# Kernel optimization log

Measured on AMD Instinct MI355X. Metric: run time of the kernel, lower is better.

The kernel has to match this reference:

```python
import jax, jax.numpy as jnp
import numpy as np

B, DIM, H, W = 2, 384, 256, 256
HID = DIM * 1          # ffn_expansion_factor = 1 (required for source code to be consistent)
P = 8                  # patch_size


def setup_inputs() -> dict:
    key = jax.random.key(0)
    k0, k1, k2, k3, k4 = jax.random.split(key, 5)
    x = jax.random.normal(k0, (B, DIM, H, W), jnp.float32)
    # learned spectral filter: (hidden, P, P//2+1), real-valued, multiplies rfft2 coeffs
    fft_filter = jax.random.normal(k1, (HID, P, P // 2 + 1), jnp.float32)
    # project_in: 1x1 conv dim->hidden, weight (out,in)
    w_in = jax.random.normal(k2, (HID, DIM), jnp.float32) * (1.0 / np.sqrt(DIM))
    # depthwise 3x3 conv, groups=channels, weight (C,1,3,3)
    w_dw = jax.random.normal(k3, (HID, 1, 3, 3), jnp.float32) * (1.0 / 3.0)
    # project_out: 1x1 conv hidden//2 -> dim
    w_out = jax.random.normal(k4, (DIM, HID // 2), jnp.float32) * (1.0 / np.sqrt(HID // 2))
    return {"x": x, "fft_filter": fft_filter, "w_in": w_in, "w_dw": w_dw, "w_out": w_out}


def reference(x, fft_filter, w_in, w_dw, w_out):
    b, c, h, w = x.shape
    hid = w_in.shape[0]
    hb, wb = h // P, w // P
    # project_in (1x1 conv == channel GEMM)
    t = jnp.einsum('bchw,oc->bohw', x, w_in)
    # patchify into 8x8 blocks and apply per-patch 2D real FFT spectral filter.
    # reshape b c (hb p1) (wb p2) -> b c hb p1 wb p2; FFT over axes (3,5).
    tp = t.reshape(b, hid, hb, P, wb, P)
    tf = jnp.fft.rfft2(tp, axes=(3, 5))                 # (b,hid,hb,P,wb,P//2+1) complex
    tf = tf * fft_filter[None, :, None, :, None, :]
    tp = jnp.fft.irfft2(tf, s=(P, P), axes=(3, 5))
    t = tp.reshape(b, hid, h, w)
    # depthwise 3x3 conv, stride 1, padding 1
    t = jax.lax.conv_general_dilated(
        t, w_dw, window_strides=(1, 1), padding='SAME',
        feature_group_count=hid,
        dimension_numbers=('NCHW', 'OIHW', 'NCHW'))
    # gated GELU (exact erf gelu, matching torch F.gelu default)
    x1, x2 = t[:, : hid // 2], t[:, hid // 2:]
    g = jax.nn.gelu(x1, approximate=False) * x2
    # project_out (1x1 conv)
    return jnp.einsum('bchw,oc->bohw', g, w_out)
```

## Files before the change

kernel.cpp:

```cpp
#include <hip/hip_runtime.h>
#include <hip/hip_bf16.h>
#include <math.h>

#define BB 2
#define DIM 384
#define HID 384
#define HW 65536

typedef short s16x8 __attribute__((ext_vector_type(8)));
typedef short s16x4 __attribute__((ext_vector_type(4)));
typedef __bf16 bf16x8 __attribute__((ext_vector_type(8)));
typedef float f32x4 __attribute__((ext_vector_type(4)));

__device__ inline short f2b(float f) {
    __hip_bfloat16 h = __float2bfloat16(f);
    return __builtin_bit_cast(short, h);
}
__device__ inline float b2f(short s) {
    return __bfloat162float(__builtin_bit_cast(__hip_bfloat16, s));
}

__device__ inline void gl_lds16(const short* g, short* l) {
    __builtin_amdgcn_global_load_lds(
        (const __attribute__((address_space(1))) unsigned int*)g,
        (__attribute__((address_space(3))) unsigned int*)l, 16, 0, 0);
}

__global__ void k_prepR(short* __restrict__ Rb) {
    int idx = blockIdx.x * 256 + threadIdx.x;
    int j = idx >> 6, k = idx & 63;
    const float cas[8] = {1.f, 1.41421356237f, 1.f, 0.f, -1.f, -1.41421356237f, -1.f, 0.f};
    int t = ((j >> 3) * (k >> 3) + (j & 7) * (k & 7)) & 7;
    Rb[idx] = f2b(cas[t]);
}

__global__ void k_prepD(const float* __restrict__ F, float* __restrict__ Dt) {
    int idx = blockIdx.x * 256 + threadIdx.x;
    int c = idx >> 6, j = idx & 63;
    int a = j >> 3, q = j & 7;
    float d;
    if (q >= 1 && q <= 3)
        d = F[c * 40 + a * 5 + q];
    else if (q >= 5)
        d = F[c * 40 + ((8 - a) & 7) * 5 + (8 - q)];
    else
        d = 0.5f * (F[c * 40 + a * 5 + q] + F[c * 40 + ((8 - a) & 7) * 5 + q]);
    Dt[j * 384 + c] = d * (1.f / 64.f);
}

__global__ void k_cvtw(const float* __restrict__ in, short* __restrict__ out, int n) {
    int i = blockIdx.x * 256 + threadIdx.x;
    if (i < n) out[i] = f2b(in[i]);
}

__global__ __launch_bounds__(256) void k_cvtx(const float* __restrict__ X, short* __restrict__ Xt) {
    int hw0 = blockIdx.x * 64, c0 = blockIdx.y * 64, b = blockIdx.z;
    __shared__ __align__(16) short S[64 * 64];
    int t = threadIdx.x;
    const float* Xb = X + ((size_t)(b * DIM) << 16);
    short* Xtb = Xt + (size_t)b * HW * DIM;
#pragma unroll
    for (int p = 0; p < 2; ++p) {
        int row = p * 32 + (t >> 3), sb = t & 7;
        const float* src = &Xb[((size_t)(c0 + row) << 16) + hw0 + sb * 8];
        float4 a = *(const float4*)src;
        float4 bq = *(const float4*)(src + 4);
        s16x8 v;
        v[0] = f2b(a.x);  v[1] = f2b(a.y);  v[2] = f2b(a.z);  v[3] = f2b(a.w);
        v[4] = f2b(bq.x); v[5] = f2b(bq.y); v[6] = f2b(bq.z); v[7] = f2b(bq.w);
        *(s16x8*)&S[row * 64 + ((sb ^ (row >> 3)) << 3)] = v;
    }
    __syncthreads();
#pragma unroll
    for (int p = 0; p < 2; ++p) {
        int row = p * 32 + (t >> 3), ch = t & 7;
        s16x8 v;
#pragma unroll
        for (int j = 0; j < 8; ++j)
            v[j] = S[(ch * 8 + j) * 64 + (row ^ (ch << 3))];
        *(s16x8*)&Xtb[(size_t)(hw0 + row) * DIM + c0 + ch * 8] = v;
    }
}

__global__ __launch_bounds__(256) void k_gemm1c(const short* __restrict__ A,
                                                const short* __restrict__ Bt,
                                                const short* __restrict__ Rb,
                                                const float* __restrict__ Dt,
                                                short* __restrict__ T) {
    __shared__ __align__(16) short SH[17408 + 4096];
    short* As = SH;
    short* Bs = SH + 4096;
    short* Rs = SH + 17408;
    int d = blockIdx.x;
    int wg = (d & 7) * 192 + (d >> 3);
    int m0 = (wg % 3) * 128;
    int tx = wg / 3;
    int h0 = (tx >> 4) * 8;
    int w0 = (tx & 15) * 16;
    int b  = blockIdx.z;
    const short* Bz = Bt + (size_t)b * HW * DIM;
    int tid = threadIdx.x;
    int lane = tid & 63, w = tid >> 6;
    int wr = w >> 1, wc = w & 1;
    int lm = lane & 15, quad = lane >> 4;

    {
        int j0 = tid >> 3, kb0 = tid & 7;
        gl_lds16(Rb + j0 * 64 + ((kb0 ^ (j0 & 7)) << 3), Rs + tid * 8);
        int t2 = tid + 256;
        int j1 = t2 >> 3, kb1 = t2 & 7;
        gl_lds16(Rb + j1 * 64 + ((kb1 ^ (j1 & 7)) << 3), Rs + t2 * 8);
    }

    f32x4 acc[4][4];
#pragma unroll
    for (int i = 0; i < 4; ++i)
#pragma unroll
        for (int j = 0; j < 4; ++j) acc[i][j] = 0.f;

    int srow = tid >> 2, sseg = tid & 3;
    int pu = srow >> 3, pv = srow & 7;
    int p1 = ((h0 + pu) << 8) + w0 + pv;
    int p2 = p1 + 8;
    for (int k0 = 0; k0 < DIM; k0 += 32) {
        gl_lds16(A + (size_t)(m0 + srow) * DIM + k0 + sseg * 8, As + tid * 8);
        gl_lds16(A + (size_t)(m0 + 64 + srow) * DIM + k0 + sseg * 8, As + (tid + 256) * 8);
        gl_lds16(Bz + (size_t)p1 * DIM + k0 + sseg * 8, Bs + tid * 8);
        gl_lds16(Bz + (size_t)p2 * DIM + k0 + sseg * 8, Bs + (tid + 256) * 8);
        __syncthreads();
        bf16x8 af[4], bfr[4];
#pragma unroll
        for (int i = 0; i < 4; ++i)
            af[i] = __builtin_bit_cast(bf16x8, *(const s16x8*)&As[(wr * 64 + i * 16 + lm) * 32 + quad * 8]);
#pragma unroll
        for (int j = 0; j < 4; ++j)
            bfr[j] = __builtin_bit_cast(bf16x8, *(const s16x8*)&Bs[(wc * 64 + j * 16 + lm) * 32 + quad * 8]);
#pragma unroll
        for (int i = 0; i < 4; ++i)
#pragma unroll
            for (int j = 0; j < 4; ++j)
                acc[i][j] = __builtin_amdgcn_mfma_f32_16x16x32_bf16(af[i], bfr[j], acc[i][j], 0, 0, 0);
        __syncthreads();
    }
#pragma unroll
    for (int i = 0; i < 4; ++i)
#pragma unroll
        for (int j = 0; j < 4; ++j)
#pragma unroll
            for (int r = 0; r < 4; ++r)
                SH[(wr * 64 + i * 16 + quad * 4 + r) * 136 + wc * 64 + j * 16 + lm] =
                    f2b(acc[i][j][r]);
    __syncthreads();

    f32x4 acc2[4][4];
#pragma unroll
    for (int i = 0; i < 4; ++i)
#pragma unroll
        for (int j = 0; j < 4; ++j) acc2[i][j] = 0.f;
#pragma unroll
    for (int ks = 0; ks < 2; ++ks) {
        bf16x8 af[4], bfr[4];
#pragma unroll
        for (int i = 0; i < 4; ++i)
            af[i] = __builtin_bit_cast(bf16x8,
                *(const s16x8*)&SH[(wr * 64 + i * 16 + lm) * 136 + wc * 64 + ks * 32 + quad * 8]);
#pragma unroll
        for (int jf = 0; jf < 4; ++jf)
            bfr[jf] = __builtin_bit_cast(bf16x8,
                *(const s16x8*)&Rs[(jf * 16 + lm) * 64 + (((ks * 4 + quad) ^ (lm & 7)) << 3)]);
#pragma unroll
        for (int i = 0; i < 4; ++i)
#pragma unroll
            for (int jf = 0; jf < 4; ++jf)
                acc2[i][jf] = __builtin_amdgcn_mfma_f32_16x16x32_bf16(af[i], bfr[jf], acc2[i][jf], 0, 0, 0);
    }
#pragma unroll
    for (int i = 0; i < 4; ++i)
#pragma unroll
        for (int jf = 0; jf < 4; ++jf) {
            int j = jf * 16 + lm;
            float4 dv = *(const float4*)&Dt[j * 384 + m0 + wr * 64 + i * 16 + quad * 4];
            acc2[i][jf][0] *= dv.x; acc2[i][jf][1] *= dv.y;
            acc2[i][jf][2] *= dv.z; acc2[i][jf][3] *= dv.w;
        }
    __syncthreads();
#pragma unroll
    for (int i = 0; i < 4; ++i)
#pragma unroll
        for (int jf = 0; jf < 4; ++jf)
#pragma unroll
            for (int r = 0; r < 4; ++r)
                SH[(wr * 64 + i * 16 + quad * 4 + r) * 136 + wc * 64 + jf * 16 + lm] =
                    f2b(acc2[i][jf][r]);
    __syncthreads();

    f32x4 acc3[4][4];
#pragma unroll
    for (int i = 0; i < 4; ++i)
#pragma unroll
        for (int j = 0; j < 4; ++j) acc3[i][j] = 0.f;
#pragma unroll
    for (int ks = 0; ks < 2; ++ks) {
        bf16x8 af[4], bfr[4];
#pragma unroll
        for (int i = 0; i < 4; ++i)
            af[i] = __builtin_bit_cast(bf16x8,
                *(const s16x8*)&SH[(wr * 64 + i * 16 + lm) * 136 + wc * 64 + ks * 32 + quad * 8]);
#pragma unroll
        for (int uf = 0; uf < 4; ++uf)
            bfr[uf] = __builtin_bit_cast(bf16x8,
                *(const s16x8*)&Rs[(uf * 16 + lm) * 64 + (((ks * 4 + quad) ^ (lm & 7)) << 3)]);
#pragma unroll
        for (int i = 0; i < 4; ++i)
#pragma unroll
            for (int uf = 0; uf < 4; ++uf)
                acc3[i][uf] = __builtin_amdgcn_mfma_f32_16x16x32_bf16(af[i], bfr[uf], acc3[i][uf], 0, 0, 0);
    }
    __syncthreads();
#pragma unroll
    for (int i = 0; i < 4; ++i)
#pragma unroll
        for (int uf = 0; uf < 4; ++uf)
#pragma unroll
            for (int r = 0; r < 4; ++r)
                SH[(wr * 64 + i * 16 + quad * 4 + r) * 136 + wc * 64 + uf * 16 + lm] =
                    f2b(acc3[i][uf][r]);
    __syncthreads();
#pragma unroll
    for (int kq = 0; kq < 8; ++kq) {
        int idx = kq * 256 + tid;
        int pat = idx & 1, ch = (idx >> 1) & 127, u = idx >> 8;
        s16x8 vv = *(const s16x8*)&SH[ch * 136 + pat * 64 + u * 8];
        *(s16x8*)&T[(((size_t)(b * HID + m0 + ch)) << 16) + ((h0 + u) << 8) + w0 + pat * 8] = vv;
    }
}

__global__ __launch_bounds__(256) void k_dwgt(const short* __restrict__ Y,
                                              const float* __restrict__ Wdw,
                                              short* __restrict__ Gt) {
    int bz = blockIdx.z;
    int b  = bz / 24;
    int cg = bz % 24;
    int c0 = cg * 8;
    int h0 = blockIdx.y * 16, w0 = blockIdx.x * 64;
    __shared__ __align__(16) short S[16][18][80];
    __shared__ float sw[16][9];
    int tid = threadIdx.x;
    if (tid < 144) {
        int p = tid / 9, j = tid % 9;
        int ch = (p < 8) ? (c0 + p) : (c0 + p - 8 + 192);
        sw[p][j] = Wdw[ch * 9 + j];
    }
    for (int t = tid; t < 2880; t += 256) {
        int v = t % 10, r = (t / 10) % 18, p = t / 180;
        int gh = h0 + r - 1;
        int gw = w0 + v * 8 - 8;
        int ch = (p < 8) ? (c0 + p) : (c0 + p - 8 + 192);
        s16x8 val = {0, 0, 0, 0, 0, 0, 0, 0};
        if (gh >= 0 && gh < 256 && gw >= 0 && gw <= 248)
            val = *(const s16x8*)&Y[((size_t)(b * HID + ch) << 16) + (gh << 8) + gw];
        *(s16x8*)&S[p][r][v * 8] = val;
    }
    __syncthreads();
    s16x8 ov[4];
#pragma unroll
    for (int it = 0; it < 4; ++it) {
        int idx = it * 256 + tid;
        int p = idx >> 7, run = idx & 127;
        int r = run >> 3, c8 = (run & 7) * 8;
        float z1[8], z2[8];
#pragma unroll
        for (int k = 0; k < 8; ++k) { z1[k] = 0.f; z2[k] = 0.f; }
#pragma unroll
        for (int i = 0; i < 3; ++i) {
            {
                s16x4 wv[4];
#pragma unroll
                for (int q = 0; q < 4; ++q) wv[q] = *(const s16x4*)&S[p][r + i][c8 + 4 + q * 4];
                float fv[10];
#pragma unroll
                for (int q = 0; q < 10; ++q) fv[q] = b2f(wv[(q + 3) >> 2][(q + 3) & 3]);
#pragma unroll
                for (int j = 0; j < 3; ++j) {
                    float wgt = sw[p][i * 3 + j];
#pragma unroll
                    for (int k = 0; k < 8; ++k) z1[k] += fv[k + j] * wgt;
                }
            }
            {
                s16x4 wv[4];
#pragma unroll
                for (int q = 0; q < 4; ++q) wv[q] = *(const s16x4*)&S[p + 8][r + i][c8 + 4 + q * 4];
                float fv[10];
#pragma unroll
                for (int q = 0; q < 10; ++q) fv[q] = b2f(wv[(q + 3) >> 2][(q + 3) & 3]);
#pragma unroll
                for (int j = 0; j < 3; ++j) {
                    float wgt = sw[p + 8][i * 3 + j];
#pragma unroll
                    for (int k = 0; k < 8; ++k) z2[k] += fv[k + j] * wgt;
                }
            }
        }
#pragma unroll
        for (int k = 0; k < 8; ++k) {
            float g = 0.5f * z1[k] * (1.f + erff(z1[k] * 0.70710678118654752f));
            ov[it][k] = f2b(g * z2[k]);
        }
    }
    __syncthreads();
    short* Ob = (short*)S;
#pragma unroll
    for (int it = 0; it < 4; ++it) {
        int idx = it * 256 + tid;
        int p = idx >> 7, run = idx & 127;
        int pos = (run >> 3) * 64 + (run & 7) * 8;
#pragma unroll
        for (int k = 0; k < 8; ++k)
            Ob[(pos + k) * 9 + p] = ov[it][k];
    }
    __syncthreads();
    short* Gb = Gt + (((size_t)(b * 24 + cg)) << 16) * 8;
#pragma unroll
    for (int it = 0; it < 4; ++it) {
        int pos = it * 256 + tid;
        int r = pos >> 6, cl = pos & 63;
        s16x8 v;
#pragma unroll
        for (int k = 0; k < 8; ++k) v[k] = Ob[pos * 9 + k];
        *(s16x8*)&Gb[(size_t)(((h0 + r) << 8) + w0 + cl) * 8] = v;
    }
}

__global__ __launch_bounds__(256) void k_gemm_bf16(const short* __restrict__ A,
                                                   const short* __restrict__ Bt,
                                                   float* __restrict__ C,
                                                   int N, int K) {
    __shared__ __align__(16) short As[128 * 32];
    __shared__ __align__(16) short Bs[128 * 32];
    const short* Bz = Bt + (size_t)blockIdx.z * (size_t)N * K;
    float* Cz = C + (size_t)blockIdx.z * (size_t)384 * N;
    int d = blockIdx.x;
    int wg = (d & 7) * 192 + (d >> 3);
    int m0 = (wg % 3) * 128;
    int n0 = (wg / 3) * 128;
    int tid = threadIdx.x;
    int lane = tid & 63, w = tid >> 6;
    int wr = w >> 1, wc = w & 1;
    int lm = lane & 15, quad = lane >> 4;

    f32x4 acc[4][4];
#pragma unroll
    for (int i = 0; i < 4; ++i)
#pragma unroll
        for (int j = 0; j < 4; ++j) acc[i][j] = 0.f;

    int srow = tid >> 2, sseg = tid & 3;
    for (int k0 = 0; k0 < K; k0 += 32) {
        gl_lds16(A + (size_t)(m0 + srow) * K + k0 + sseg * 8, As + tid * 8);
        gl_lds16(A + (size_t)(m0 + 64 + srow) * K + k0 + sseg * 8, As + (tid + 256) * 8);
        gl_lds16(Bz + ((size_t)((k0 >> 3) + sseg) * HW + n0 + srow) * 8, Bs + tid * 8);
        gl_lds16(Bz + ((size_t)((k0 >> 3) + sseg) * HW + n0 + 64 + srow) * 8, Bs + (tid + 256) * 8);
        __syncthreads();
        bf16x8 af[4], bfr[4];
#pragma unroll
        for (int i = 0; i < 4; ++i)
            af[i] = __builtin_bit_cast(bf16x8, *(const s16x8*)&As[(wr * 64 + i * 16 + lm) * 32 + quad * 8]);
#pragma unroll
        for (int j = 0; j < 4; ++j)
            bfr[j] = __builtin_bit_cast(bf16x8, *(const s16x8*)&Bs[(wc * 64 + j * 16 + lm) * 32 + quad * 8]);
#pragma unroll
        for (int i = 0; i < 4; ++i)
#pragma unroll
            for (int j = 0; j < 4; ++j)
                acc[i][j] = __builtin_amdgcn_mfma_f32_16x16x32_bf16(af[i], bfr[j], acc[i][j], 0, 0, 0);
        __syncthreads();
    }
#pragma unroll
    for (int i = 0; i < 4; ++i) {
        int r0 = m0 + wr * 64 + i * 16 + quad * 4;
#pragma unroll
        for (int j = 0; j < 4; ++j) {
            int cidx = n0 + wc * 64 + j * 16 + lm;
#pragma unroll
            for (int r = 0; r < 4; ++r)
                Cz[(size_t)(r0 + r) * N + cidx] = acc[i][j][r];
        }
    }
}

extern "C" void kernel_launch(void* const* d_in, const int* in_sizes, int n_in,
                              void* d_out, int out_size, void* d_ws, size_t ws_size,
                              hipStream_t stream) {
    const float* x     = (const float*)d_in[0];
    const float* ff    = (const float*)d_in[1];
    const float* w_in  = (const float*)d_in[2];
    const float* w_dw  = (const float*)d_in[3];
    const float* w_out = (const float*)d_in[4];
    float* out = (float*)d_out;

    char* ws = (char*)d_ws;
    float* Dt   = (float*)ws;
    short* wbin = (short*)(ws + 98304);
    short* wbout = (short*)(ws + 393216);
    short* Rbuf = (short*)(ws + 540672);
    short* bufA = (short*)(ws + 548864);
    short* bufB = (short*)(ws + 548864 + (size_t)100663296);
    short* Gt = bufA;

    k_prepR<<<16, 256, 0, stream>>>(Rbuf);
    k_prepD<<<96, 256, 0, stream>>>(ff, Dt);
    k_cvtw<<<(DIM * DIM + 255) / 256, 256, 0, stream>>>(w_in, wbin, DIM * DIM);
    k_cvtw<<<(DIM * 192 + 255) / 256, 256, 0, stream>>>(w_out, wbout, DIM * 192);
    k_cvtx<<<dim3(HW / 64, DIM / 64, BB), 256, 0, stream>>>(x, bufA);

    k_gemm1c<<<dim3(1536, 1, BB), 256, 0, stream>>>(wbin, bufA, Rbuf, Dt, bufB);

    k_dwgt<<<dim3(4, 16, BB * 24), 256, 0, stream>>>(bufB, w_dw, Gt);

    k_gemm_bf16<<<dim3(1536, 1, BB), 256, 0, stream>>>(wbout, Gt, out, HW, 192);
}
```

Measured before the change: 599.6 us.

## Store filtered intermediate patch-major, drop intra-warp barriers, merge prep kernels

The spectral-filter GEMM kernel now writes its bf16 output in a patch-major layout (each 8x8 patch contiguous), so every channel row's store is one contiguous 256-byte run. The depthwise-conv kernel's loads are re-indexed to match. Four __syncthreads between the staged MFMA passes are removed, because each warp only reads back the shared-memory tile region it wrote itself. The four small weight and table prep kernels are merged into one launch to cut launch overhead. The risk is that the halo loads in the depthwise kernel now come from scattered patch rows, which may reduce coalescing there.

```diff
diff --git a/kernel.cpp b/kernel.cpp
--- a/kernel.cpp
+++ b/kernel.cpp
@@ -26,31 +26,35 @@
         (__attribute__((address_space(3))) unsigned int*)l, 16, 0, 0);
 }
 
-__global__ void k_prepR(short* __restrict__ Rb) {
-    int idx = blockIdx.x * 256 + threadIdx.x;
-    int j = idx >> 6, k = idx & 63;
-    const float cas[8] = {1.f, 1.41421356237f, 1.f, 0.f, -1.f, -1.41421356237f, -1.f, 0.f};
-    int t = ((j >> 3) * (k >> 3) + (j & 7) * (k & 7)) & 7;
-    Rb[idx] = f2b(cas[t]);
-}
-
-__global__ void k_prepD(const float* __restrict__ F, float* __restrict__ Dt) {
-    int idx = blockIdx.x * 256 + threadIdx.x;
-    int c = idx >> 6, j = idx & 63;
-    int a = j >> 3, q = j & 7;
-    float d;
-    if (q >= 1 && q <= 3)
-        d = F[c * 40 + a * 5 + q];
-    else if (q >= 5)
-        d = F[c * 40 + ((8 - a) & 7) * 5 + (8 - q)];
-    else
-        d = 0.5f * (F[c * 40 + a * 5 + q] + F[c * 40 + ((8 - a) & 7) * 5 + q]);
-    Dt[j * 384 + c] = d * (1.f / 64.f);
-}
-
-__global__ void k_cvtw(const float* __restrict__ in, short* __restrict__ out, int n) {
+__global__ void k_prep(const float* __restrict__ w_in, const float* __restrict__ w_out,
+                       const float* __restrict__ F,
+                       short* __restrict__ wbin, short* __restrict__ wbout,
+                       float* __restrict__ Dt, short* __restrict__ Rb) {
     int i = blockIdx.x * 256 + threadIdx.x;
-    if (i < n) out[i] = f2b(in[i]);
+    if (i < 147456) { wbin[i] = f2b(w_in[i]); return; }
+    i -= 147456;
+    if (i < 73728) { wbout[i] = f2b(w_out[i]); return; }
+    i -= 73728;
+    if (i < 24576) {
+        int c = i >> 6, j = i & 63;
+        int a = j >> 3, q = j & 7;
+        float d;
+        if (q >= 1 && q <= 3)
+            d = F[c * 40 + a * 5 + q];
+        else if (q >= 5)
+            d = F[c * 40 + ((8 - a) & 7) * 5 + (8 - q)];
+        else
+            d = 0.5f * (F[c * 40 + a * 5 + q] + F[c * 40 + ((8 - a) & 7) * 5 + q]);
+        Dt[j * 384 + c] = d * (1.f / 64.f);
+        return;
+    }
+    i -= 24576;
+    if (i < 4096) {
+        int j = i >> 6, k = i & 63;
+        const float cas[8] = {1.f, 1.41421356237f, 1.f, 0.f, -1.f, -1.41421356237f, -1.f, 0.f};
+        int t = ((j >> 3) * (k >> 3) + (j & 7) * (k & 7)) & 7;
+        Rb[i] = f2b(cas[t]);
+    }
 }
 
 __global__ __launch_bounds__(256) void k_cvtx(const float* __restrict__ X, short* __restrict__ Xt) {
@@ -150,7 +154,6 @@
             for (int r = 0; r < 4; ++r)
                 SH[(wr * 64 + i * 16 + quad * 4 + r) * 136 + wc * 64 + j * 16 + lm] =
                     f2b(acc[i][j][r]);
-    __syncthreads();
 
     f32x4 acc2[4][4];
 #pragma unroll
@@ -183,7 +186,6 @@
             acc2[i][jf][0] *= dv.x; acc2[i][jf][1] *= dv.y;
             acc2[i][jf][2] *= dv.z; acc2[i][jf][3] *= dv.w;
         }
-    __syncthreads();
 #pragma unroll
     for (int i = 0; i < 4; ++i)
 #pragma unroll
@@ -192,7 +194,6 @@
             for (int r = 0; r < 4; ++r)
                 SH[(wr * 64 + i * 16 + quad * 4 + r) * 136 + wc * 64 + jf * 16 + lm] =
                     f2b(acc2[i][jf][r]);
-    __syncthreads();
 
     f32x4 acc3[4][4];
 #pragma unroll
@@ -216,7 +217,6 @@
             for (int uf = 0; uf < 4; ++uf)
                 acc3[i][uf] = __builtin_amdgcn_mfma_f32_16x16x32_bf16(af[i], bfr[uf], acc3[i][uf], 0, 0, 0);
     }
-    __syncthreads();
 #pragma unroll
     for (int i = 0; i < 4; ++i)
 #pragma unroll
@@ -226,12 +226,13 @@
                 SH[(wr * 64 + i * 16 + quad * 4 + r) * 136 + wc * 64 + uf * 16 + lm] =
                     f2b(acc3[i][uf][r]);
     __syncthreads();
+    int pid0 = (h0 >> 3) * 32 + (w0 >> 3);
 #pragma unroll
     for (int kq = 0; kq < 8; ++kq) {
         int idx = kq * 256 + tid;
-        int pat = idx & 1, ch = (idx >> 1) & 127, u = idx >> 8;
-        s16x8 vv = *(const s16x8*)&SH[ch * 136 + pat * 64 + u * 8];
-        *(s16x8*)&T[(((size_t)(b * HID + m0 + ch)) << 16) + ((h0 + u) << 8) + w0 + pat * 8] = vv;
+        int row = idx >> 4, seg = idx & 15;
+        s16x8 vv = *(const s16x8*)&SH[row * 136 + seg * 8];
+        *(s16x8*)&T[(((size_t)(b * HID + m0 + row)) << 16) + (pid0 << 6) + seg * 8] = vv;
     }
 }
 
@@ -257,8 +258,10 @@
         int gw = w0 + v * 8 - 8;
         int ch = (p < 8) ? (c0 + p) : (c0 + p - 8 + 192);
         s16x8 val = {0, 0, 0, 0, 0, 0, 0, 0};
-        if (gh >= 0 && gh < 256 && gw >= 0 && gw <= 248)
-            val = *(const s16x8*)&Y[((size_t)(b * HID + ch) << 16) + (gh << 8) + gw];
+        if (gh >= 0 && gh < 256 && gw >= 0 && gw <= 248) {
+            int pid = ((gh >> 3) << 5) + (gw >> 3);
+            val = *(const s16x8*)&Y[((size_t)(b * HID + ch) << 16) + (pid << 6) + ((gh & 7) << 3)];
+        }
         *(s16x8*)&S[p][r][v * 8] = val;
     }
     __syncthreads();
@@ -408,10 +411,7 @@
     short* bufB = (short*)(ws + 548864 + (size_t)100663296);
     short* Gt = bufA;
 
-    k_prepR<<<16, 256, 0, stream>>>(Rbuf);
-    k_prepD<<<96, 256, 0, stream>>>(ff, Dt);
-    k_cvtw<<<(DIM * DIM + 255) / 256, 256, 0, stream>>>(w_in, wbin, DIM * DIM);
-    k_cvtw<<<(DIM * 192 + 255) / 256, 256, 0, stream>>>(w_out, wbout, DIM * 192);
+    k_prep<<<976, 256, 0, stream>>>(w_in, w_out, ff, wbin, wbout, Dt, Rbuf);
     k_cvtx<<<dim3(HW / 64, DIM / 64, BB), 256, 0, stream>>>(x, bufA);
 
     k_gemm1c<<<dim3(1536, 1, BB), 256, 0, stream>>>(wbin, bufA, Rbuf, Dt, bufB);
```

After: 585.7 us. -2.3%, faster.
